# Kernel tuning notes

Hardware: AMD Instinct MI355X
Metric: run time of the kernel (lower is better)

The kernel has to match this reference:

```python
import jax, jax.numpy as jnp
import numpy as np

N_HEAD = 12
HEAD_SIZE = 64  # 768 / 12
SCALE = 1.0 / np.sqrt(HEAD_SIZE)


def setup_inputs() -> dict:
    key = jax.random.key(0)
    k1, k2, k3 = jax.random.split(key, 3)
    B, T, C = 8, 1024, 768
    x = jax.random.normal(k1, (B, T, C), dtype=jnp.float32)
    W_attn = jax.random.normal(k2, (C, 3 * C), dtype=jnp.float32) * 0.02
    b_attn = jax.random.normal(k3, (3 * C,), dtype=jnp.float32) * 0.02
    return {"x": x, "W_attn": W_attn, "b_attn": b_attn}


def reference(x, W_attn, b_attn):
    B, T, C = x.shape
    hs = C // N_HEAD
    qkv = x @ W_attn + b_attn                      # [B, T, 3C]
    q, k, v = jnp.split(qkv, 3, axis=-1)
    # [B, nh, T, hs]
    q = q.reshape(B, T, N_HEAD, hs).transpose(0, 2, 1, 3)
    k = k.reshape(B, T, N_HEAD, hs).transpose(0, 2, 1, 3)
    v = v.reshape(B, T, N_HEAD, hs).transpose(0, 2, 1, 3)
    scores = jnp.einsum('bhqd,bhkd->bhqk', q, k) * SCALE
    causal = jnp.tril(jnp.ones((T, T), dtype=bool))  # [T, T]
    # masked positions get -inf then relu -> 0; equivalent to where(mask, relu, 0)
    att = jnp.where(causal, jax.nn.relu(scores), 0.0)
    y = jnp.einsum('bhqk,bhkd->bhqd', att, v)      # [B, nh, T, hs]
    return y.transpose(0, 2, 1, 3).reshape(B, T, C)
```

## Files before the change

kernel.cpp:

```cpp
#include <hip/hip_runtime.h>
#include <stdint.h>

typedef __bf16 bf16;
typedef __attribute__((ext_vector_type(8))) __bf16 bf16x8;
typedef __attribute__((ext_vector_type(4))) __bf16 bf16x4;
typedef __attribute__((ext_vector_type(4))) float  f32x4;

#define ATT_SCALE 0.125f

__device__ __forceinline__ void async16(void* lds, const void* g) {
  __builtin_amdgcn_global_load_lds(
      (__attribute__((address_space(1))) void*)(void*)g,
      (__attribute__((address_space(3))) void*)lds,
      16, 0, 0);
}

__global__ void convert_x_kernel(const float* __restrict__ x, bf16* __restrict__ y) {
  size_t i = ((size_t)blockIdx.x * 256 + threadIdx.x) * 8;
  float4 a = *(const float4*)(x + i);
  float4 b = *(const float4*)(x + i + 4);
  bf16x8 o;
  o[0] = (bf16)a.x; o[1] = (bf16)a.y; o[2] = (bf16)a.z; o[3] = (bf16)a.w;
  o[4] = (bf16)b.x; o[5] = (bf16)b.y; o[6] = (bf16)b.z; o[7] = (bf16)b.w;
  *(bf16x8*)(y + i) = o;
}

__global__ void transpose_w_kernel(const float* __restrict__ W, bf16* __restrict__ Wt) {
  __shared__ float tile[32][33];
  int tx = threadIdx.x, ty = threadIdx.y;
  int n0 = blockIdx.x * 32, k0 = blockIdx.y * 32;
#pragma unroll
  for (int r = 0; r < 4; ++r)
    tile[ty + r * 8][tx] = W[(size_t)(k0 + ty + r * 8) * 2304 + n0 + tx];
  __syncthreads();
#pragma unroll
  for (int r = 0; r < 4; ++r)
    Wt[(size_t)(n0 + ty + r * 8) * 768 + k0 + tx] = (bf16)tile[tx][ty + r * 8];
}

__global__ void qkv_gemm_kernel(const bf16* __restrict__ A, const bf16* __restrict__ Bw,
                                const float* __restrict__ bias,
                                bf16* __restrict__ Qo, bf16* __restrict__ Ko,
                                bf16* __restrict__ Vo) {
  __shared__ __align__(16) char lds[65536];

  const int tid  = threadIdx.x;
  const int wave = tid >> 6, lane = tid & 63;
  const int quad = lane >> 4, mn = lane & 15;
  const int wr = wave >> 1, wc = wave & 1;
  const int m0 = blockIdx.y * 128;
  const int n0 = blockIdx.x * 128;

  f32x4 acc[4][4] = {};

  const int lrow = lane >> 3;
  const int cg   = (lane & 7) ^ lrow;

  auto stage = [&](int kt, char* buf) {
    char* Al = buf;
    char* Bl = buf + 16384;
#pragma unroll
    for (int u = 0; u < 4; ++u) {
      const int t   = wave * 4 + u;
      const int row = t * 8 + lrow;
      async16(Al + t * 1024 + lane * 16,
              A  + (size_t)(m0 + row) * 768 + kt + cg * 8);
      async16(Bl + t * 1024 + lane * 16,
              Bw + (size_t)(n0 + row) * 768 + kt + cg * 8);
    }
  };

  stage(0, lds);
  int p = 0;
  for (int kt = 0; kt < 768; kt += 64) {
    __syncthreads();
    if (kt + 64 < 768) stage(kt + 64, lds + (p ^ 1) * 32768);
    char* Al = lds + p * 32768;
    char* Bl = Al + 16384;

#pragma unroll
    for (int s = 0; s < 2; ++s) {
      bf16x8 af[4], bfr[4];
      const int csw = ((s * 4 + quad) ^ (mn & 7)) * 16;
#pragma unroll
      for (int i = 0; i < 4; ++i) {
        af[i]  = *(const bf16x8*)(Al + (wr * 64 + i * 16 + mn) * 128 + csw);
        bfr[i] = *(const bf16x8*)(Bl + (wc * 64 + i * 16 + mn) * 128 + csw);
      }
#pragma unroll
      for (int i = 0; i < 4; ++i)
#pragma unroll
        for (int j = 0; j < 4; ++j)
          acc[i][j] = __builtin_amdgcn_mfma_f32_16x16x32_bf16(af[i], bfr[j], acc[i][j], 0, 0, 0);
    }
    p ^= 1;
  }

  const int ng    = n0 + wc * 64;
  const int third = ng / 768;
  const int nmod  = ng % 768;
  const float sc  = (third == 0) ? ATT_SCALE : 1.0f;
#pragma unroll
  for (int ct = 0; ct < 4; ++ct) {
    int n = nmod + ct * 16 + mn;
    int h = n >> 6, d = n & 63;
    float bv = bias[third * 768 + n];
#pragma unroll
    for (int rt = 0; rt < 4; ++rt) {
      int m  = m0 + wr * 64 + rt * 16 + quad * 4;
      int b  = m >> 10, t0 = m & 1023;
      size_t bh = (size_t)b * 12 + h;
      if (third == 2) {
        bf16x4 pk;
#pragma unroll
        for (int r = 0; r < 4; ++r) pk[r] = (bf16)(acc[rt][ct][r] + bv);
        *(bf16x4*)(Vo + (bh * 64 + d) * 1024 + t0) = pk;
      } else {
        bf16* dst = (third == 0 ? Qo : Ko) + (bh * 1024 + t0) * 64 + d;
#pragma unroll
        for (int r = 0; r < 4; ++r) dst[(size_t)r * 64] = (bf16)((acc[rt][ct][r] + bv) * sc);
      }
    }
  }
}

__global__ __launch_bounds__(256, 4)
void attn_kernel(const bf16* __restrict__ Q, const bf16* __restrict__ K,
                 const bf16* __restrict__ Vt, float* __restrict__ out) {
  __shared__ __align__(16) char lds[36864];
  char* ldsK = lds;
  char* ldsV = lds + 9216;
  char* ldsS = lds + 18432;

  const int tid  = threadIdx.x;
  const int wave = tid >> 6, lane = tid & 63;
  const int quad = lane >> 4, mn = lane & 15;
  const int bh  = blockIdx.x;
  const int qta = blockIdx.y;
  const int qtb = 15 - qta;
  const int qa0 = qta * 64, qb0 = qtb * 64;

  const bf16* Qg  = Q  + (size_t)bh * 65536;
  const bf16* Kg0 = K  + (size_t)bh * 65536;
  const bf16* Vg0 = Vt + (size_t)bh * 65536;

  bf16x8 qfA[2], qfB[2];
  {
    const bf16* ra = Qg + (size_t)(qa0 + wave * 16 + mn) * 64;
    qfA[0] = *(const bf16x8*)(ra + quad * 8);
    qfA[1] = *(const bf16x8*)(ra + 32 + quad * 8);
    const bf16* rb = Qg + (size_t)(qb0 + wave * 16 + mn) * 64;
    qfB[0] = *(const bf16x8*)(rb + quad * 8);
    qfB[1] = *(const bf16x8*)(rb + 32 + quad * 8);
  }

  f32x4 yA[4] = {}, yB[4] = {};

  const int trow = tid >> 3;
  const int tcol = tid & 7;

  bf16x8 r0 = *(const bf16x8*)(Kg0 + trow * 64 + tcol * 8);
  bf16x8 r1 = *(const bf16x8*)(Kg0 + (trow + 32) * 64 + tcol * 8);
  bf16x8 r2 = *(const bf16x8*)(Vg0 + (size_t)trow * 1024 + tcol * 8);
  bf16x8 r3 = *(const bf16x8*)(Vg0 + (size_t)(trow + 32) * 1024 + tcol * 8);

  for (int j = 0; j <= qtb; ++j) {
    if (j) __syncthreads();
    *(bf16x8*)(ldsK + trow * 144 + tcol * 16) = r0;
    *(bf16x8*)(ldsK + (trow + 32) * 144 + tcol * 16) = r1;
    *(bf16x8*)(ldsV + trow * 144 + tcol * 16) = r2;
    *(bf16x8*)(ldsV + (trow + 32) * 144 + tcol * 16) = r3;
    __syncthreads();
    if (j < qtb) {
      const bf16* Kg = Kg0 + (size_t)(j + 1) * 4096;
      const bf16* Vg = Vg0 + (j + 1) * 64;
      r0 = *(const bf16x8*)(Kg + trow * 64 + tcol * 8);
      r1 = *(const bf16x8*)(Kg + (trow + 32) * 64 + tcol * 8);
      r2 = *(const bf16x8*)(Vg + (size_t)trow * 1024 + tcol * 8);
      r3 = *(const bf16x8*)(Vg + (size_t)(trow + 32) * 1024 + tcol * 8);
    }

    auto do_half = [&](const bf16x8* qf, f32x4* y, int half, int qrow0, bool diag) {
#pragma unroll
      for (int ct = 0; ct < 4; ++ct) {
        bf16x8 kf0 = *(const bf16x8*)(ldsK + (ct * 16 + mn) * 144 + quad * 16);
        bf16x8 kf1 = *(const bf16x8*)(ldsK + (ct * 16 + mn) * 144 + 64 + quad * 16);
        f32x4 a = {};
        a = __builtin_amdgcn_mfma_f32_16x16x32_bf16(qf[0], kf0, a, 0, 0, 0);
        a = __builtin_amdgcn_mfma_f32_16x16x32_bf16(qf[1], kf1, a, 0, 0, 0);
        int kkc = j * 64 + ct * 16 + mn;
#pragma unroll
        for (int r = 0; r < 4; ++r) {
          float v = a[r];
          v = v > 0.f ? v : 0.f;
          if (diag && kkc > qrow0 + quad * 4 + r) v = 0.f;
          ((bf16*)ldsS)[(half * 64 + wave * 16 + quad * 4 + r) * 72 + ct * 16 + mn] = (bf16)v;
        }
      }
#pragma unroll
      for (int kb = 0; kb < 2; ++kb) {
        bf16x8 sf = *(const bf16x8*)(ldsS + (half * 64 + wave * 16 + mn) * 144 + kb * 64 + quad * 16);
#pragma unroll
        for (int ct = 0; ct < 4; ++ct) {
          bf16x8 vf = *(const bf16x8*)(ldsV + (ct * 16 + mn) * 144 + kb * 64 + quad * 16);
          y[ct] = __builtin_amdgcn_mfma_f32_16x16x32_bf16(sf, vf, y[ct], 0, 0, 0);
        }
      }
    };

    if (j <= qta) do_half(qfA, yA, 0, qa0 + wave * 16, j == qta);
    do_half(qfB, yB, 1, qb0 + wave * 16, j == qtb);
  }

  const int b = bh / 12, h = bh % 12;
  {
    float* ob = out + ((size_t)b * 1024 + qa0 + wave * 16 + quad * 4) * 768 + h * 64;
#pragma unroll
    for (int ct = 0; ct < 4; ++ct)
#pragma unroll
      for (int r = 0; r < 4; ++r)
        ob[(size_t)r * 768 + ct * 16 + mn] = yA[ct][r];
  }
  {
    float* ob = out + ((size_t)b * 1024 + qb0 + wave * 16 + quad * 4) * 768 + h * 64;
#pragma unroll
    for (int ct = 0; ct < 4; ++ct)
#pragma unroll
      for (int r = 0; r < 4; ++r)
        ob[(size_t)r * 768 + ct * 16 + mn] = yB[ct][r];
  }
}

extern "C" void kernel_launch(void* const* d_in, const int* in_sizes, int n_in,
                              void* d_out, int out_size, void* d_ws, size_t ws_size,
                              hipStream_t stream) {
  const float* x    = (const float*)d_in[0];
  const float* W    = (const float*)d_in[1];
  const float* bias = (const float*)d_in[2];
  float* out = (float*)d_out;

  char* ws = (char*)d_ws;
  bf16* xb = (bf16*)(ws);
  bf16* Wt = (bf16*)(ws + 12582912);
  bf16* Qb = (bf16*)(ws + 16121856);
  bf16* Kb = (bf16*)(ws + 28704768);
  bf16* Vb = (bf16*)(ws + 41287680);

  convert_x_kernel<<<3072, 256, 0, stream>>>(x, xb);
  transpose_w_kernel<<<dim3(72, 24), dim3(32, 8), 0, stream>>>(W, Wt);
  qkv_gemm_kernel<<<dim3(18, 64), 256, 0, stream>>>(xb, Wt, bias, Qb, Kb, Vb);
  attn_kernel<<<dim3(96, 8), 256, 0, stream>>>(Qb, Kb, Vb, out);
}
```

Before: 152.7 us.

## Double-buffer attention K/V tiles via async LDS loads and hoist fragments

Replaces the register-staged K/V prefetch in the attention kernel with direct global-to-LDS async loads into a double-buffered, XOR-swizzled layout. K and V fragments are read into registers once per tile and reused for both query halves. The score MFMA operands are swapped so each lane writes a packed 4-wide bf16 store to LDS instead of four scalar stores. This raises LDS use and register pressure, so the launch bound drops from 4 to 3 blocks per SIMD, which may reduce occupancy.

Result: no change. 149.7 us (-1.9%).

```diff
diff --git a/kernel.cpp b/kernel.cpp
--- a/kernel.cpp
+++ b/kernel.cpp
@@ -124,13 +124,11 @@
   }
 }
 
-__global__ __launch_bounds__(256, 4)
+__global__ __launch_bounds__(256, 3)
 void attn_kernel(const bf16* __restrict__ Q, const bf16* __restrict__ K,
                  const bf16* __restrict__ Vt, float* __restrict__ out) {
-  __shared__ __align__(16) char lds[36864];
-  char* ldsK = lds;
-  char* ldsV = lds + 9216;
-  char* ldsS = lds + 18432;
+  __shared__ __align__(16) char lds[51200];
+  char* ldsS = lds + 32768;
 
   const int tid  = threadIdx.x;
   const int wave = tid >> 6, lane = tid & 63;
@@ -156,60 +154,67 @@
 
   f32x4 yA[4] = {}, yB[4] = {};
 
-  const int trow = tid >> 3;
-  const int tcol = tid & 7;
-
-  bf16x8 r0 = *(const bf16x8*)(Kg0 + trow * 64 + tcol * 8);
-  bf16x8 r1 = *(const bf16x8*)(Kg0 + (trow + 32) * 64 + tcol * 8);
-  bf16x8 r2 = *(const bf16x8*)(Vg0 + (size_t)trow * 1024 + tcol * 8);
-  bf16x8 r3 = *(const bf16x8*)(Vg0 + (size_t)(trow + 32) * 1024 + tcol * 8);
-
+  const int lrow = lane >> 3;
+  const int cg   = (lane & 7) ^ lrow;
+
+  auto stageKV = [&](int j, char* buf) {
+#pragma unroll
+    for (int u2 = 0; u2 < 2; ++u2) {
+      const int u   = wave * 2 + u2;
+      const int row = u * 8 + lrow;
+      async16(buf + u * 1024 + lane * 16,
+              Kg0 + (size_t)(j * 64 + row) * 64 + cg * 8);
+      async16(buf + 8192 + u * 1024 + lane * 16,
+              Vg0 + (size_t)row * 1024 + j * 64 + cg * 8);
+    }
+  };
+
+  stageKV(0, lds);
   for (int j = 0; j <= qtb; ++j) {
-    if (j) __syncthreads();
-    *(bf16x8*)(ldsK + trow * 144 + tcol * 16) = r0;
-    *(bf16x8*)(ldsK + (trow + 32) * 144 + tcol * 16) = r1;
-    *(bf16x8*)(ldsV + trow * 144 + tcol * 16) = r2;
-    *(bf16x8*)(ldsV + (trow + 32) * 144 + tcol * 16) = r3;
     __syncthreads();
-    if (j < qtb) {
-      const bf16* Kg = Kg0 + (size_t)(j + 1) * 4096;
-      const bf16* Vg = Vg0 + (j + 1) * 64;
-      r0 = *(const bf16x8*)(Kg + trow * 64 + tcol * 8);
-      r1 = *(const bf16x8*)(Kg + (trow + 32) * 64 + tcol * 8);
-      r2 = *(const bf16x8*)(Vg + (size_t)trow * 1024 + tcol * 8);
-      r3 = *(const bf16x8*)(Vg + (size_t)(trow + 32) * 1024 + tcol * 8);
-    }
-
-    auto do_half = [&](const bf16x8* qf, f32x4* y, int half, int qrow0, bool diag) {
+    if (j < qtb) stageKV(j + 1, lds + ((j + 1) & 1) * 16384);
+    char* bK = lds + (j & 1) * 16384;
+    char* bV = bK + 8192;
+
+    bf16x8 kf[4][2], vf[4][2];
+    const int sw = mn & 7;
+#pragma unroll
+    for (int ct = 0; ct < 4; ++ct) {
+      const int ro = (ct * 16 + mn) * 128;
+      kf[ct][0] = *(const bf16x8*)(bK + ro + ((quad)     ^ sw) * 16);
+      kf[ct][1] = *(const bf16x8*)(bK + ro + ((4 + quad) ^ sw) * 16);
+      vf[ct][0] = *(const bf16x8*)(bV + ro + ((quad)     ^ sw) * 16);
+      vf[ct][1] = *(const bf16x8*)(bV + ro + ((4 + quad) ^ sw) * 16);
+    }
+
+    auto do_half = [&](const bf16x8* qf, f32x4* y, int half, int qrow, bool diag) {
 #pragma unroll
       for (int ct = 0; ct < 4; ++ct) {
-        bf16x8 kf0 = *(const bf16x8*)(ldsK + (ct * 16 + mn) * 144 + quad * 16);
-        bf16x8 kf1 = *(const bf16x8*)(ldsK + (ct * 16 + mn) * 144 + 64 + quad * 16);
         f32x4 a = {};
-        a = __builtin_amdgcn_mfma_f32_16x16x32_bf16(qf[0], kf0, a, 0, 0, 0);
-        a = __builtin_amdgcn_mfma_f32_16x16x32_bf16(qf[1], kf1, a, 0, 0, 0);
-        int kkc = j * 64 + ct * 16 + mn;
+        a = __builtin_amdgcn_mfma_f32_16x16x32_bf16(kf[ct][0], qf[0], a, 0, 0, 0);
+        a = __builtin_amdgcn_mfma_f32_16x16x32_bf16(kf[ct][1], qf[1], a, 0, 0, 0);
+        const int kkg = j * 64 + ct * 16 + quad * 4;
+        bf16x4 pk;
 #pragma unroll
         for (int r = 0; r < 4; ++r) {
           float v = a[r];
           v = v > 0.f ? v : 0.f;
-          if (diag && kkc > qrow0 + quad * 4 + r) v = 0.f;
-          ((bf16*)ldsS)[(half * 64 + wave * 16 + quad * 4 + r) * 72 + ct * 16 + mn] = (bf16)v;
+          if (diag && kkg + r > qrow) v = 0.f;
+          pk[r] = (bf16)v;
         }
+        *(bf16x4*)(ldsS + (half * 64 + wave * 16 + mn) * 144 + (ct * 16 + quad * 4) * 2) = pk;
       }
 #pragma unroll
       for (int kb = 0; kb < 2; ++kb) {
         bf16x8 sf = *(const bf16x8*)(ldsS + (half * 64 + wave * 16 + mn) * 144 + kb * 64 + quad * 16);
 #pragma unroll
-        for (int ct = 0; ct < 4; ++ct) {
-          bf16x8 vf = *(const bf16x8*)(ldsV + (ct * 16 + mn) * 144 + kb * 64 + quad * 16);
-          y[ct] = __builtin_amdgcn_mfma_f32_16x16x32_bf16(sf, vf, y[ct], 0, 0, 0);
-        }
+        for (int ct = 0; ct < 4; ++ct)
+          y[ct] = __builtin_amdgcn_mfma_f32_16x16x32_bf16(sf, vf[ct][kb], y[ct], 0, 0, 0);
       }
     };
 
-    if (j <= qta) do_half(qfA, yA, 0, qa0 + wave * 16, j == qta);
-    do_half(qfB, yB, 1, qb0 + wave * 16, j == qtb);
+    if (j <= qta) do_half(qfA, yA, 0, qa0 + wave * 16 + mn, j == qta);
+    do_half(qfB, yB, 1, qb0 + wave * 16 + mn, j == qtb);
   }
 
   const int b = bh / 12, h = bh % 12;
```
